# Performance work log

Measured on AMD Instinct MI355X. Metric: run time of the kernel, lower is better.

The kernel has to match this reference:

```python
import jax, jax.numpy as jnp
import numpy as np

DIM = 1024
HIDDEN = 2048
NUM_EXPERTS = 8
TOP_K = 2


def setup_inputs() -> dict:
    key = jax.random.key(0)
    ks = jax.random.split(key, 6)
    scale = 0.02
    x = jax.random.normal(ks[0], (2, 4096, DIM), dtype=jnp.float32)
    # router: Linear(dim, num_experts, bias=False) -> weight [E, d]
    router_w = jax.random.normal(ks[1], (NUM_EXPERTS, DIM), dtype=jnp.float32) * scale
    # per-expert MLP: Linear(d, h) -> w1 [E, h, d], b1 [E, h]; Linear(h, d) -> w2 [E, d, h], b2 [E, d]
    w1 = jax.random.normal(ks[2], (NUM_EXPERTS, HIDDEN, DIM), dtype=jnp.float32) * scale
    b1 = jnp.zeros((NUM_EXPERTS, HIDDEN), dtype=jnp.float32)
    w2 = jax.random.normal(ks[3], (NUM_EXPERTS, DIM, HIDDEN), dtype=jnp.float32) * scale
    b2 = jnp.zeros((NUM_EXPERTS, DIM), dtype=jnp.float32)
    return {"x": x, "router_w": router_w, "w1": w1, "b1": b1, "w2": w2, "b2": b2}


def reference(x, router_w, w1, b1, w2, b2):
    b, s, d = x.shape
    xf = x.reshape(-1, d)                              # [T, d]
    logits = xf @ router_w.T                           # [T, E]
    all_probs = jax.nn.softmax(logits, axis=-1)
    topk_logits, topk_inds = jax.lax.top_k(logits, TOP_K)   # [T, K]
    topk_probs = jax.nn.softmax(topk_logits, axis=-1)
    E = router_w.shape[0]
    onehot = jax.nn.one_hot(topk_inds, E, dtype=xf.dtype)   # [T, K, E]
    # combine weights per (token, expert); zero where expert not selected
    gate = jnp.einsum('tke,tk->te', onehot, topk_probs)     # [T, E]
    # load-balancing auxiliary loss
    f_i = onehot.mean(axis=(0, 1))                          # [E]
    P_i = all_probs.mean(axis=0)                            # [E]
    aux_loss = E * jnp.sum(f_i * P_i)
    # dense per-expert MLP, weighted combine (dropout=0 / eval mode)
    out = jnp.zeros_like(xf)
    for e in range(E):  # fixed small loop over experts
        h = jax.nn.gelu(xf @ w1[e].T + b1[e], approximate=False)  # exact GELU (torch default)
        y = h @ w2[e].T + b2[e]
        out = out + gate[:, e:e + 1] * y
    return out.reshape(b, s, d), aux_loss
```

## Files before the change

kernel.cpp:

```cpp
#include <hip/hip_runtime.h>


#define TOKS 8192
#define DIMD 1024
#define HID  2048
#define NE   8

#define OFF_COUNTS   0
#define OFF_OFFSETS  64
#define OFF_CURSORS  128
#define OFF_TILEOFF  192
#define OFF_TOPKI    256
#define OFF_TOPKG    (OFF_TOPKI + TOKS*2*4)
#define OFF_BLKPS    (OFF_TOPKG + TOKS*2*4)
#define OFF_ATOK     (OFF_BLKPS + 2048*NE*4)
#define OFF_AGATE    (OFF_ATOK + TOKS*2*4)
#define OFF_PINV     (OFF_AGATE + TOKS*2*4)
#define OFF_XG       (1u << 20)
#define XG_ROWS      (TOKS*2 + 256)
#define OFF_W1B      (OFF_XG  + (size_t)XG_ROWS * DIMD * 2)
#define OFF_W2B      (OFF_W1B + (size_t)NE * HID * DIMD * 2)
#define OFF_H        (OFF_W2B + (size_t)NE * DIMD * HID * 2)
#define OFF_Y        (OFF_H   + (size_t)XG_ROWS * HID * 2)

typedef __bf16 bf16x8 __attribute__((ext_vector_type(8)));
typedef float  floatx4 __attribute__((ext_vector_type(4)));

__device__ __forceinline__ float bf2f(unsigned short u) {
    return __uint_as_float(((unsigned)u) << 16);
}
__device__ __forceinline__ unsigned short f2bf(float f) {
    unsigned u = __float_as_uint(f);
    unsigned r = (u + 0x7FFFu + ((u >> 16) & 1u)) >> 16;
    return (unsigned short)r;
}

#define GLOBAL_AS(p) ((const __attribute__((address_space(1))) unsigned int*)(p))
#define LDS_AS(p)    ((__attribute__((address_space(3))) unsigned int*)(p))

__device__ __forceinline__ int xcd_remap(int bid, int nwg) {
    int xcd = bid & 7, pos = bid >> 3;
    int q = nwg >> 3, r = nwg & 7;
    int start = (xcd < r) ? xcd * (q + 1) : r * (q + 1) + (xcd - r) * q;
    return start + pos;
}

__global__ void convert_w_kernel(const float4* __restrict__ w1,
                                 ushort4* __restrict__ w1b, int n1,
                                 const float4* __restrict__ w2,
                                 ushort4* __restrict__ w2b, int n2) {
    int i = blockIdx.x * blockDim.x + threadIdx.x;
    int stride = gridDim.x * blockDim.x;
    int ntot = n1 + n2;
    for (; i < ntot; i += stride) {
        float4 v; ushort4 o;
        if (i < n1) v = w1[i]; else v = w2[i - n1];
        o.x = f2bf(v.x); o.y = f2bf(v.y); o.z = f2bf(v.z); o.w = f2bf(v.w);
        if (i < n1) w1b[i] = o; else w2b[i - n1] = o;
    }
}

__global__ __launch_bounds__(256) void router_kernel(
    const float* __restrict__ x, const float* __restrict__ rw,
    int* __restrict__ topki, float* __restrict__ topkg,
    float* __restrict__ blkps)
{
    int wave = threadIdx.x >> 6;
    int lane = threadIdx.x & 63;
    int t = blockIdx.x * 4 + wave;
    const float* xt = x + (size_t)t * DIMD;

    float acc[NE];
#pragma unroll
    for (int e = 0; e < NE; e++) acc[e] = 0.f;
    for (int i = 0; i < DIMD / 64; i++) {
        float xv = xt[lane + 64 * i];
#pragma unroll
        for (int e = 0; e < NE; e++) acc[e] += xv * rw[e * DIMD + lane + 64 * i];
    }
#pragma unroll
    for (int off = 32; off > 0; off >>= 1) {
#pragma unroll
        for (int e = 0; e < NE; e++) acc[e] += __shfl_down(acc[e], off);
    }

    __shared__ float ps[4][NE];
    if (lane == 0) {
        float m = acc[0];
#pragma unroll
        for (int e = 1; e < NE; e++) m = fmaxf(m, acc[e]);
        float ex[NE], s = 0.f;
#pragma unroll
        for (int e = 0; e < NE; e++) { ex[e] = expf(acc[e] - m); s += ex[e]; }
        float inv = 1.f / s;
#pragma unroll
        for (int e = 0; e < NE; e++) ps[wave][e] = ex[e] * inv;

        int i0 = 0; float l0 = acc[0];
#pragma unroll
        for (int e = 1; e < NE; e++) if (acc[e] > l0) { l0 = acc[e]; i0 = e; }
        int i1 = -1; float l1 = -3.4e38f;
#pragma unroll
        for (int e = 0; e < NE; e++) if (e != i0 && acc[e] > l1) { l1 = acc[e]; i1 = e; }
        float e1 = expf(l1 - l0);
        float g0 = 1.f / (1.f + e1);
        float g1 = e1 * g0;
        topki[t * 2 + 0] = i0; topki[t * 2 + 1] = i1;
        topkg[t * 2 + 0] = g0; topkg[t * 2 + 1] = g1;
    }
    __syncthreads();
    if (threadIdx.x < NE) {
        float s = ps[0][threadIdx.x] + ps[1][threadIdx.x] + ps[2][threadIdx.x] + ps[3][threadIdx.x];
        blkps[blockIdx.x * NE + threadIdx.x] = s;
    }
}

__global__ __launch_bounds__(256) void finalize_kernel(
    const int* __restrict__ topki, const float* __restrict__ blkps,
    int* __restrict__ counts, int* __restrict__ offsets, int* __restrict__ cursors,
    int* __restrict__ tileoff, float* __restrict__ aux_out)
{
    __shared__ float psum[NE];
    __shared__ int cnt[NE];
    int tid = threadIdx.x;
    if (tid < NE) { psum[tid] = 0.f; cnt[tid] = 0; }
    __syncthreads();

    float lp[NE]; int lc[NE];
#pragma unroll
    for (int e = 0; e < NE; e++) { lp[e] = 0.f; lc[e] = 0; }
    const float4* bp4 = (const float4*)blkps;
    for (int i = tid; i < 2048 * NE / 4; i += 256) {
        float4 v = bp4[i];
        int eb = (4 * i) & 7;
        lp[eb + 0] += v.x; lp[eb + 1] += v.y; lp[eb + 2] += v.z; lp[eb + 3] += v.w;
    }
    const int4* ti4 = (const int4*)topki;
    for (int i = tid; i < TOKS * 2 / 4; i += 256) {
        int4 v = ti4[i];
        lc[v.x]++; lc[v.y]++; lc[v.z]++; lc[v.w]++;
    }
#pragma unroll
    for (int e = 0; e < NE; e++) { atomicAdd(&psum[e], lp[e]); atomicAdd(&cnt[e], lc[e]); }
    __syncthreads();

    if (tid == 0) {
        int off = 0, to = 0;
        for (int e = 0; e < NE; e++) {
            counts[e] = cnt[e];
            offsets[e] = off; cursors[e] = off;
            tileoff[e] = to;
            off += cnt[e];
            to += (cnt[e] + 255) >> 8;
        }
        offsets[NE] = off; tileoff[NE] = to;
        float aux = 0.f;
        for (int e = 0; e < NE; e++)
            aux += ((float)cnt[e] / (float)(TOKS * 2)) * (psum[e] / (float)TOKS);
        aux_out[0] = (float)NE * aux;
    }
}

__global__ __launch_bounds__(64) void fill_kernel(
    const int* __restrict__ topki, const float* __restrict__ topkg,
    int* __restrict__ cursors, int* __restrict__ atok, float* __restrict__ agate,
    int* __restrict__ posinv)
{
    int lane = threadIdx.x;
    int t = blockIdx.x * 64 + lane;
    unsigned long long below = (lane == 63) ? 0x7FFFFFFFFFFFFFFFull
                                            : ((1ull << lane) - 1ull);
#pragma unroll
    for (int k = 0; k < 2; k++) {
        int e = topki[t * 2 + k];
        float g = topkg[t * 2 + k];
        for (int ee = 0; ee < NE; ee++) {
            bool pred = (e == ee);
            unsigned long long mask = __ballot(pred ? 1 : 0);
            if (mask) {
                int leader = __ffsll((unsigned long long)mask) - 1;
                int base = 0;
                if (lane == leader) base = atomicAdd(&cursors[ee], (int)__popcll(mask));
                base = __shfl(base, leader);
                if (pred) {
                    int pos = base + (int)__popcll(mask & below);
                    atok[pos] = t;
                    agate[pos] = g;
                    posinv[t * 2 + k] = pos;
                }
            }
        }
    }
}

__global__ __launch_bounds__(256) void gather_x_kernel(
    const float* __restrict__ x, const int* __restrict__ atok,
    ushort* __restrict__ Xg)
{
    int r = blockIdx.x;
    int tid = threadIdx.x;
    int tok = atok[r];
    float4 v = ((const float4*)(x + (size_t)tok * DIMD))[tid];
    ushort4 o;
    o.x = f2bf(v.x); o.y = f2bf(v.y); o.z = f2bf(v.z); o.w = f2bf(v.w);
    ((ushort4*)(Xg + (size_t)r * DIMD))[tid] = o;
}

template<int LD, int NT>
__device__ __forceinline__ void gemm8ph(
    const ushort* __restrict__ gApanel, const ushort* __restrict__ gBpanel,
    ushort (&lds)[2][64][512], floatx4 (&acc)[8][4],
    int lane, int wave, int wr, int wc, int l15, int quad)
{
    const bf16x8* C0 = (const bf16x8*)&lds[0][0][0];
    const bf16x8* C1 = (const bf16x8*)&lds[1][0][0];

    auto stage_half = [&](int bsel, int hf, int u) {
        const ushort* panel = (hf & 2) ? gBpanel : gApanel;
        int rbase = (hf & 1) * 128 + wave * 16 + l15;
        const ushort* s0 = panel + (size_t)rbase * LD + u * 64 + quad * 8;
        __builtin_amdgcn_global_load_lds(GLOBAL_AS(s0),
            LDS_AS(&lds[bsel][hf * 16 + wave * 2 + 0][0]), 16, 0, 0);
        __builtin_amdgcn_global_load_lds(GLOBAL_AS(s0 + 32),
            LDS_AS(&lds[bsel][hf * 16 + wave * 2 + 1][0]), 16, 0, 0);
    };

#pragma unroll
    for (int i = 0; i < 8; i++)
#pragma unroll
        for (int j = 0; j < 4; j++) acc[i][j] = (floatx4){0.f, 0.f, 0.f, 0.f};

    bf16x8 af[4][2], bf[2][2];

#define PH(CB, MH, NH, RA, RB, DOSTAGE, SB, SHF, SU, DOWAIT, DEEP)            \
    {                                                                          \
        if (RA) {                                                              \
            _Pragma("unroll") for (int mi = 0; mi < 4; mi++) {                 \
                af[mi][0] = CB[((wr * 8 + (MH)*4 + mi) * 2 + 0) * 64 + lane];  \
                af[mi][1] = CB[((wr * 8 + (MH)*4 + mi) * 2 + 1) * 64 + lane];  \
            }                                                                  \
        }                                                                      \
        if (RB) {                                                              \
            _Pragma("unroll") for (int nj = 0; nj < 2; nj++) {                 \
                bf[nj][0] = CB[(32 + (wc * 4 + (NH)*2 + nj) * 2 + 0) * 64 + lane]; \
                bf[nj][1] = CB[(32 + (wc * 4 + (NH)*2 + nj) * 2 + 1) * 64 + lane]; \
            }                                                                  \
        }                                                                      \
        if (DOSTAGE) stage_half(SB, SHF, SU);                                  \
        __builtin_amdgcn_s_barrier();                                          \
        asm volatile("s_waitcnt lgkmcnt(0)" ::: "memory");                     \
        __builtin_amdgcn_sched_barrier(0);                                     \
        __builtin_amdgcn_s_setprio(1);                                         \
        _Pragma("unroll") for (int mi = 0; mi < 4; mi++)                       \
            _Pragma("unroll") for (int nj = 0; nj < 2; nj++)                   \
                _Pragma("unroll") for (int kk = 0; kk < 2; kk++)               \
                    acc[(MH)*4 + mi][(NH)*2 + nj] =                            \
                        __builtin_amdgcn_mfma_f32_16x16x32_bf16(               \
                            af[mi][kk], bf[nj][kk],                            \
                            acc[(MH)*4 + mi][(NH)*2 + nj], 0, 0, 0);           \
        __builtin_amdgcn_s_setprio(0);                                         \
        if (DOWAIT) {                                                          \
            if (DEEP) asm volatile("s_waitcnt vmcnt(0)" ::: "memory");         \
            else      asm volatile("s_waitcnt vmcnt(4)" ::: "memory");         \
        }                                                                      \
        __builtin_amdgcn_s_barrier();                                          \
    }

    stage_half(0, 0, 0);
    stage_half(0, 2, 0);
    stage_half(0, 3, 0);
    stage_half(0, 1, 0);
    stage_half(1, 0, 1);
    stage_half(1, 3, 1);
    asm volatile("s_waitcnt vmcnt(4)" ::: "memory");
    __builtin_amdgcn_s_barrier();

    for (int u = 0; u < NT; u += 2) {
        PH(C0, 0, 0, 1, 1, (u + 1 < NT), 1, 1, u + 1, 0, 0);
        PH(C0, 0, 1, 0, 1, (u + 1 < NT), 1, 2, u + 1, 0, 0);
        PH(C0, 1, 1, 1, 0, (u + 2 < NT), 0, 0, u + 2, 0, 0);
        PH(C0, 1, 0, 0, 1, (u + 2 < NT), 0, 3, u + 2, 1, (u + 2 >= NT));
        PH(C1, 0, 0, 1, 1, (u + 2 < NT), 0, 1, u + 2, 0, 0);
        PH(C1, 0, 1, 0, 1, (u + 2 < NT), 0, 2, u + 2, 0, 0);
        PH(C1, 1, 1, 1, 0, (u + 3 < NT), 1, 0, u + 3, 0, 0);
        PH(C1, 1, 0, 0, 1, (u + 3 < NT), 1, 3, u + 3, 1, (u + 3 >= NT));
    }
#undef PH
}

__global__ __launch_bounds__(512, 2) void phase1_kernel(
    const ushort* __restrict__ Xg, const ushort* __restrict__ w1b,
    const float* __restrict__ b1,
    const int* __restrict__ counts, const int* __restrict__ offsets,
    const int* __restrict__ tileoff, unsigned short* __restrict__ Hbuf)
{
    const int NCOLT = HID / 256;
    int total = tileoff[NE] * NCOLT;
    int idx = xcd_remap((int)blockIdx.x, (int)gridDim.x);
    if (idx >= total) return;
    int ct = idx & (NCOLT - 1);
    int rowt = idx / NCOLT;
    int e = 0;
    while (rowt >= tileoff[e + 1]) e++;
    int row0 = (rowt - tileoff[e]) * 256;
    int cnt = counts[e];
    int base = offsets[e];
    int colbase = ct * 256;

    __shared__ ushort lds[2][64][512];

    int tid = threadIdx.x;
    int lane = tid & 63;
    int wave = tid >> 6;
    int wr = wave >> 2, wc = wave & 3;
    int l15 = lane & 15, quad = lane >> 4;

    const ushort* gApanel = Xg + (size_t)(base + row0) * DIMD;
    const ushort* gBpanel = w1b + (size_t)e * HID * DIMD + (size_t)colbase * DIMD;

    floatx4 acc[8][4];
    gemm8ph<DIMD, DIMD / 64>(gApanel, gBpanel, lds, acc, lane, wave, wr, wc, l15, quad);

    float b1v[4];
#pragma unroll
    for (int j = 0; j < 4; j++)
        b1v[j] = b1[e * HID + colbase + 64 * wc + 16 * j + l15];
#pragma unroll
    for (int i = 0; i < 8; i++) {
#pragma unroll
        for (int rr = 0; rr < 4; rr++) {
            int pr = row0 + 128 * wr + 16 * i + quad * 4 + rr;
            if (pr < cnt) {
                size_t hrow = (size_t)(base + pr) * HID;
#pragma unroll
                for (int j = 0; j < 4; j++) {
                    int col = colbase + 64 * wc + 16 * j + l15;
                    float v = acc[i][j][rr] + b1v[j];
                    v = 0.5f * v * (1.f + erff(v * 0.70710678118654752f));
                    Hbuf[hrow + col] = f2bf(v);
                }
            }
        }
    }
}

__global__ __launch_bounds__(512, 2) void phase2_kernel(
    const ushort* __restrict__ Hbuf, const ushort* __restrict__ w2b,
    const int* __restrict__ counts, const int* __restrict__ offsets,
    const int* __restrict__ tileoff, ushort* __restrict__ Y)
{
    const int NCOLT = DIMD / 256;
    int total = tileoff[NE] * NCOLT;
    int idx = xcd_remap((int)blockIdx.x, (int)gridDim.x);
    if (idx >= total) return;
    int ct = idx & (NCOLT - 1);
    int rowt = idx / NCOLT;
    int e = 0;
    while (rowt >= tileoff[e + 1]) e++;
    int row0 = (rowt - tileoff[e]) * 256;
    int cnt = counts[e];
    int base = offsets[e];
    int colbase = ct * 256;

    __shared__ ushort lds[2][64][512];

    int tid = threadIdx.x;
    int lane = tid & 63;
    int wave = tid >> 6;
    int wr = wave >> 2, wc = wave & 3;
    int l15 = lane & 15, quad = lane >> 4;

    const ushort* gApanel = Hbuf + (size_t)(base + row0) * HID;
    const ushort* gBpanel = w2b + (size_t)e * DIMD * HID + (size_t)colbase * HID;

    floatx4 acc[8][4];
    gemm8ph<HID, HID / 64>(gApanel, gBpanel, lds, acc, lane, wave, wr, wc, l15, quad);

#pragma unroll
    for (int i = 0; i < 8; i++) {
#pragma unroll
        for (int rr = 0; rr < 4; rr++) {
            int pr = row0 + 128 * wr + 16 * i + quad * 4 + rr;
            if (pr < cnt) {
                size_t yrow = (size_t)(base + pr) * DIMD;
#pragma unroll
                for (int j = 0; j < 4; j++) {
                    int col = colbase + 64 * wc + 16 * j + l15;
                    Y[yrow + col] = f2bf(acc[i][j][rr]);
                }
            }
        }
    }
}

__global__ __launch_bounds__(256) void combine_kernel(
    const ushort* __restrict__ Y, const float* __restrict__ b2,
    const int* __restrict__ topki, const float* __restrict__ topkg,
    const int* __restrict__ posinv, float* __restrict__ out)
{
    int wave = threadIdx.x >> 6;
    int lane = threadIdx.x & 63;
    int t = blockIdx.x * 4 + wave;
    int e0 = topki[t * 2 + 0], e1 = topki[t * 2 + 1];
    float g0 = topkg[t * 2 + 0], g1 = topkg[t * 2 + 1];
    int p0 = posinv[t * 2 + 0], p1 = posinv[t * 2 + 1];

    const ushort4* y0 = (const ushort4*)(Y + (size_t)p0 * DIMD);
    const ushort4* y1 = (const ushort4*)(Y + (size_t)p1 * DIMD);
    const float4* b20 = (const float4*)(b2 + (size_t)e0 * DIMD);
    const float4* b21 = (const float4*)(b2 + (size_t)e1 * DIMD);
    float4* o4 = (float4*)(out + (size_t)t * DIMD);

#pragma unroll
    for (int c = 0; c < DIMD / 4 / 64; c++) {
        int i = lane + 64 * c;
        ushort4 a = y0[i], b = y1[i];
        float4 ba = b20[i], bb = b21[i];
        float4 r;
        r.x = g0 * (bf2f(a.x) + ba.x) + g1 * (bf2f(b.x) + bb.x);
        r.y = g0 * (bf2f(a.y) + ba.y) + g1 * (bf2f(b.y) + bb.y);
        r.z = g0 * (bf2f(a.z) + ba.z) + g1 * (bf2f(b.z) + bb.z);
        r.w = g0 * (bf2f(a.w) + ba.w) + g1 * (bf2f(b.w) + bb.w);
        o4[i] = r;
    }
}

extern "C" void kernel_launch(void* const* d_in, const int* in_sizes, int n_in,
                              void* d_out, int out_size, void* d_ws, size_t ws_size,
                              hipStream_t stream) {
    const float* x  = (const float*)d_in[0];
    const float* rw = (const float*)d_in[1];
    const float* w1 = (const float*)d_in[2];
    const float* b1 = (const float*)d_in[3];
    const float* w2 = (const float*)d_in[4];
    const float* b2 = (const float*)d_in[5];
    float* out = (float*)d_out;

    char* ws = (char*)d_ws;
    int*   counts  = (int*)(ws + OFF_COUNTS);
    int*   offsets = (int*)(ws + OFF_OFFSETS);
    int*   cursors = (int*)(ws + OFF_CURSORS);
    int*   tileoff = (int*)(ws + OFF_TILEOFF);
    int*   topki   = (int*)(ws + OFF_TOPKI);
    float* topkg   = (float*)(ws + OFF_TOPKG);
    float* blkps   = (float*)(ws + OFF_BLKPS);
    int*   atok    = (int*)(ws + OFF_ATOK);
    float* agate   = (float*)(ws + OFF_AGATE);
    int*   posinv  = (int*)(ws + OFF_PINV);
    ushort* Xg     = (ushort*)(ws + OFF_XG);
    ushort* w1b    = (ushort*)(ws + OFF_W1B);
    ushort* w2b    = (ushort*)(ws + OFF_W2B);
    ushort* Hbuf   = (ushort*)(ws + OFF_H);
    ushort* Y      = (ushort*)(ws + OFF_Y);

    convert_w_kernel<<<8192, 256, 0, stream>>>(
        (const float4*)w1, (ushort4*)w1b, NE * HID * DIMD / 4,
        (const float4*)w2, (ushort4*)w2b, NE * DIMD * HID / 4);

    router_kernel<<<TOKS / 4, 256, 0, stream>>>(x, rw, topki, topkg, blkps);
    finalize_kernel<<<1, 256, 0, stream>>>(topki, blkps, counts, offsets, cursors,
                                           tileoff, out + (size_t)TOKS * DIMD);
    fill_kernel<<<TOKS / 64, 64, 0, stream>>>(topki, topkg, cursors, atok, agate,
                                              posinv);
    gather_x_kernel<<<TOKS * 2, 256, 0, stream>>>(x, atok, Xg);

    phase1_kernel<<<71 * (HID / 256), 512, 0, stream>>>(
        Xg, w1b, b1, counts, offsets, tileoff, Hbuf);
    phase2_kernel<<<71 * (DIMD / 256), 512, 0, stream>>>(
        Hbuf, w2b, counts, offsets, tileoff, Y);
    combine_kernel<<<TOKS / 4, 256, 0, stream>>>(Y, b2, topki, topkg, posinv, out);
}
```

Baseline: 591.3 us.

## Restage GEMM LDS loads by fragment units to prefetch deeper and drop lgkm waits

Changes how the 8-phase bf16 MFMA GEMM stages A/B tiles into LDS. Tiles are now staged in fragment-aligned units, so each phase's prefetch frees and refills exactly the rows it finished consuming. One more unit is prefetched up front (vmcnt 4→6), and the explicit lgkmcnt(0) wait and sched_barrier before the MFMAs are replaced with compiler memory fences. This aims to overlap global loads with compute more deeply and cut stall points, at the risk of LDS read/write hazards if the new unit ordering or wait counts are wrong.

Result: no change. 582.2 us (-1.5%).

```diff
diff --git a/kernel.cpp b/kernel.cpp
--- a/kernel.cpp
+++ b/kernel.cpp
@@ -37,6 +37,7 @@
 
 #define GLOBAL_AS(p) ((const __attribute__((address_space(1))) unsigned int*)(p))
 #define LDS_AS(p)    ((__attribute__((address_space(3))) unsigned int*)(p))
+#define CFENCE()     asm volatile("" ::: "memory")
 
 __device__ __forceinline__ int xcd_remap(int bid, int nwg) {
     int xcd = bid & 7, pos = bid >> 3;
@@ -215,14 +216,23 @@
     const bf16x8* C0 = (const bf16x8*)&lds[0][0][0];
     const bf16x8* C1 = (const bf16x8*)&lds[1][0][0];
 
-    auto stage_half = [&](int bsel, int hf, int u) {
-        const ushort* panel = (hf & 2) ? gBpanel : gApanel;
-        int rbase = (hf & 1) * 128 + wave * 16 + l15;
-        const ushort* s0 = panel + (size_t)rbase * LD + u * 64 + quad * 8;
+    auto stage_unit = [&](int bsel, int unit, int u) {
+        int s, chunk;
+        const ushort* panel;
+        if (unit < 2) {
+            s = (wave < 4 ? wave : wave + 4) + unit * 4;
+            chunk = s * 2;
+            panel = gApanel;
+        } else {
+            s = (wave & 1) + ((wave >> 1) * 4) + ((unit == 3) ? 2 : 0);
+            chunk = 32 + s * 2;
+            panel = gBpanel;
+        }
+        const ushort* s0 = panel + (size_t)(s * 16 + l15) * LD + u * 64 + quad * 8;
         __builtin_amdgcn_global_load_lds(GLOBAL_AS(s0),
-            LDS_AS(&lds[bsel][hf * 16 + wave * 2 + 0][0]), 16, 0, 0);
+            LDS_AS(&lds[bsel][chunk + 0][0]), 16, 0, 0);
         __builtin_amdgcn_global_load_lds(GLOBAL_AS(s0 + 32),
-            LDS_AS(&lds[bsel][hf * 16 + wave * 2 + 1][0]), 16, 0, 0);
+            LDS_AS(&lds[bsel][chunk + 1][0]), 16, 0, 0);
     };
 
 #pragma unroll
@@ -232,24 +242,24 @@
 
     bf16x8 af[4][2], bf[2][2];
 
-#define PH(CB, MH, NH, RA, RB, DOSTAGE, SB, SHF, SU, DOWAIT, DEEP)            \
+#define PH(CB, MH, NH, RA, RB, DOSTAGE, SB, SUNIT, SU, DOWAIT, DEEP)          \
     {                                                                          \
+        if (RB) {                                                              \
+            _Pragma("unroll") for (int nj = 0; nj < 2; nj++) {                 \
+                bf[nj][0] = CB[(32 + (wc * 4 + (NH)*2 + nj) * 2 + 0) * 64 + lane]; \
+                bf[nj][1] = CB[(32 + (wc * 4 + (NH)*2 + nj) * 2 + 1) * 64 + lane]; \
+            }                                                                  \
+        }                                                                      \
         if (RA) {                                                              \
             _Pragma("unroll") for (int mi = 0; mi < 4; mi++) {                 \
                 af[mi][0] = CB[((wr * 8 + (MH)*4 + mi) * 2 + 0) * 64 + lane];  \
                 af[mi][1] = CB[((wr * 8 + (MH)*4 + mi) * 2 + 1) * 64 + lane];  \
             }                                                                  \
         }                                                                      \
-        if (RB) {                                                              \
-            _Pragma("unroll") for (int nj = 0; nj < 2; nj++) {                 \
-                bf[nj][0] = CB[(32 + (wc * 4 + (NH)*2 + nj) * 2 + 0) * 64 + lane]; \
-                bf[nj][1] = CB[(32 + (wc * 4 + (NH)*2 + nj) * 2 + 1) * 64 + lane]; \
-            }                                                                  \
-        }                                                                      \
-        if (DOSTAGE) stage_half(SB, SHF, SU);                                  \
+        if (DOSTAGE) stage_unit(SB, SUNIT, SU);                                \
+        CFENCE();                                                              \
         __builtin_amdgcn_s_barrier();                                          \
-        asm volatile("s_waitcnt lgkmcnt(0)" ::: "memory");                     \
-        __builtin_amdgcn_sched_barrier(0);                                     \
+        CFENCE();                                                              \
         __builtin_amdgcn_s_setprio(1);                                         \
         _Pragma("unroll") for (int mi = 0; mi < 4; mi++)                       \
             _Pragma("unroll") for (int nj = 0; nj < 2; nj++)                   \
@@ -261,29 +271,34 @@
         __builtin_amdgcn_s_setprio(0);                                         \
         if (DOWAIT) {                                                          \
             if (DEEP) asm volatile("s_waitcnt vmcnt(0)" ::: "memory");         \
-            else      asm volatile("s_waitcnt vmcnt(4)" ::: "memory");         \
+            else      asm volatile("s_waitcnt vmcnt(6)" ::: "memory");         \
         }                                                                      \
+        CFENCE();                                                              \
         __builtin_amdgcn_s_barrier();                                          \
-    }
-
-    stage_half(0, 0, 0);
-    stage_half(0, 2, 0);
-    stage_half(0, 3, 0);
-    stage_half(0, 1, 0);
-    stage_half(1, 0, 1);
-    stage_half(1, 3, 1);
-    asm volatile("s_waitcnt vmcnt(4)" ::: "memory");
+        CFENCE();                                                              \
+    }
+
+    stage_unit(0, 0, 0);
+    stage_unit(0, 2, 0);
+    stage_unit(0, 3, 0);
+    stage_unit(0, 1, 0);
+    stage_unit(1, 0, 1);
+    stage_unit(1, 3, 1);
+    stage_unit(1, 1, 1);
+    asm volatile("s_waitcnt vmcnt(6)" ::: "memory");
+    CFENCE();
     __builtin_amdgcn_s_barrier();
+    CFENCE();
 
     for (int u = 0; u < NT; u += 2) {
-        PH(C0, 0, 0, 1, 1, (u + 1 < NT), 1, 1, u + 1, 0, 0);
-        PH(C0, 0, 1, 0, 1, (u + 1 < NT), 1, 2, u + 1, 0, 0);
-        PH(C0, 1, 1, 1, 0, (u + 2 < NT), 0, 0, u + 2, 0, 0);
-        PH(C0, 1, 0, 0, 1, (u + 2 < NT), 0, 3, u + 2, 1, (u + 2 >= NT));
-        PH(C1, 0, 0, 1, 1, (u + 2 < NT), 0, 1, u + 2, 0, 0);
-        PH(C1, 0, 1, 0, 1, (u + 2 < NT), 0, 2, u + 2, 0, 0);
-        PH(C1, 1, 1, 1, 0, (u + 3 < NT), 1, 0, u + 3, 0, 0);
-        PH(C1, 1, 0, 0, 1, (u + 3 < NT), 1, 3, u + 3, 1, (u + 3 >= NT));
+        PH(C0, 0, 0, 1, 1, (u + 1 < NT), 1, 2, u + 1, 0, 0);
+        PH(C0, 0, 1, 0, 1, (u + 2 < NT), 0, 0, u + 2, 0, 0);
+        PH(C0, 1, 1, 1, 0, (u + 2 < NT), 0, 3, u + 2, 0, 0);
+        PH(C0, 1, 0, 0, 1, (u + 2 < NT), 0, 1, u + 2, 1, (u + 2 >= NT));
+        PH(C1, 0, 0, 1, 1, (u + 2 < NT), 0, 2, u + 2, 0, 0);
+        PH(C1, 0, 1, 0, 1, (u + 3 < NT), 1, 0, u + 3, 0, 0);
+        PH(C1, 1, 1, 1, 0, (u + 3 < NT), 1, 3, u + 3, 0, 0);
+        PH(C1, 1, 0, 0, 1, (u + 3 < NT), 1, 1, u + 3, 1, (u + 3 >= NT));
     }
 #undef PH
 }
```

## Replace 8-phase GEMM pipeline with one fat phase per K-tile

Applied to the files above, without the earlier changes.

Replaces the eight-phase ping-pong schedule, where LDS fragment reads, half-tile staging and MFMA bursts were interleaved with a barrier pair per phase, with a simpler loop. Each K-tile now reads all A and B fragments at once, issues the full stage of tile u+2, then runs 64 MFMAs. This cuts the number of barriers per K-tile from 16 to 2 and lengthens the MFMA bursts. In exchange it needs more fragment registers (8x2 + 4x2 bf16x8), which puts the launch bound of 2 blocks per CU at risk. It also loses the finer overlap between LDS reads and compute across the two waves.

Result: no change. 593.1 us (+0.3%).

```diff
diff --git a/kernel.cpp b/kernel.cpp
--- a/kernel.cpp
+++ b/kernel.cpp
@@ -207,22 +207,26 @@
 }
 
 template<int LD, int NT>
-__device__ __forceinline__ void gemm8ph(
+__device__ __forceinline__ void gemm_fat(
     const ushort* __restrict__ gApanel, const ushort* __restrict__ gBpanel,
     ushort (&lds)[2][64][512], floatx4 (&acc)[8][4],
     int lane, int wave, int wr, int wc, int l15, int quad)
 {
-    const bf16x8* C0 = (const bf16x8*)&lds[0][0][0];
-    const bf16x8* C1 = (const bf16x8*)&lds[1][0][0];
-
-    auto stage_half = [&](int bsel, int hf, int u) {
-        const ushort* panel = (hf & 2) ? gBpanel : gApanel;
-        int rbase = (hf & 1) * 128 + wave * 16 + l15;
-        const ushort* s0 = panel + (size_t)rbase * LD + u * 64 + quad * 8;
-        __builtin_amdgcn_global_load_lds(GLOBAL_AS(s0),
-            LDS_AS(&lds[bsel][hf * 16 + wave * 2 + 0][0]), 16, 0, 0);
-        __builtin_amdgcn_global_load_lds(GLOBAL_AS(s0 + 32),
-            LDS_AS(&lds[bsel][hf * 16 + wave * 2 + 1][0]), 16, 0, 0);
+    auto stage_tile = [&](int bsel, int u) {
+#pragma unroll
+        for (int t = 0; t < 2; t++) {
+            int s = wave * 2 + t;
+            const ushort* a0 = gApanel + (size_t)(s * 16 + l15) * LD + u * 64 + quad * 8;
+            __builtin_amdgcn_global_load_lds(GLOBAL_AS(a0),
+                LDS_AS(&lds[bsel][s * 2 + 0][0]), 16, 0, 0);
+            __builtin_amdgcn_global_load_lds(GLOBAL_AS(a0 + 32),
+                LDS_AS(&lds[bsel][s * 2 + 1][0]), 16, 0, 0);
+            const ushort* b0 = gBpanel + (size_t)(s * 16 + l15) * LD + u * 64 + quad * 8;
+            __builtin_amdgcn_global_load_lds(GLOBAL_AS(b0),
+                LDS_AS(&lds[bsel][32 + s * 2 + 0][0]), 16, 0, 0);
+            __builtin_amdgcn_global_load_lds(GLOBAL_AS(b0 + 32),
+                LDS_AS(&lds[bsel][32 + s * 2 + 1][0]), 16, 0, 0);
+        }
     };
 
 #pragma unroll
@@ -230,62 +234,48 @@
 #pragma unroll
         for (int j = 0; j < 4; j++) acc[i][j] = (floatx4){0.f, 0.f, 0.f, 0.f};
 
-    bf16x8 af[4][2], bf[2][2];
-
-#define PH(CB, MH, NH, RA, RB, DOSTAGE, SB, SHF, SU, DOWAIT, DEEP)            \
-    {                                                                          \
-        if (RA) {                                                              \
-            _Pragma("unroll") for (int mi = 0; mi < 4; mi++) {                 \
-                af[mi][0] = CB[((wr * 8 + (MH)*4 + mi) * 2 + 0) * 64 + lane];  \
-                af[mi][1] = CB[((wr * 8 + (MH)*4 + mi) * 2 + 1) * 64 + lane];  \
-            }                                                                  \
-        }                                                                      \
-        if (RB) {                                                              \
-            _Pragma("unroll") for (int nj = 0; nj < 2; nj++) {                 \
-                bf[nj][0] = CB[(32 + (wc * 4 + (NH)*2 + nj) * 2 + 0) * 64 + lane]; \
-                bf[nj][1] = CB[(32 + (wc * 4 + (NH)*2 + nj) * 2 + 1) * 64 + lane]; \
-            }                                                                  \
-        }                                                                      \
-        if (DOSTAGE) stage_half(SB, SHF, SU);                                  \
-        __builtin_amdgcn_s_barrier();                                          \
-        asm volatile("s_waitcnt lgkmcnt(0)" ::: "memory");                     \
-        __builtin_amdgcn_sched_barrier(0);                                     \
-        __builtin_amdgcn_s_setprio(1);                                         \
-        _Pragma("unroll") for (int mi = 0; mi < 4; mi++)                       \
-            _Pragma("unroll") for (int nj = 0; nj < 2; nj++)                   \
-                _Pragma("unroll") for (int kk = 0; kk < 2; kk++)               \
-                    acc[(MH)*4 + mi][(NH)*2 + nj] =                            \
-                        __builtin_amdgcn_mfma_f32_16x16x32_bf16(               \
-                            af[mi][kk], bf[nj][kk],                            \
-                            acc[(MH)*4 + mi][(NH)*2 + nj], 0, 0, 0);           \
-        __builtin_amdgcn_s_setprio(0);                                         \
-        if (DOWAIT) {                                                          \
-            if (DEEP) asm volatile("s_waitcnt vmcnt(0)" ::: "memory");         \
-            else      asm volatile("s_waitcnt vmcnt(4)" ::: "memory");         \
-        }                                                                      \
-        __builtin_amdgcn_s_barrier();                                          \
-    }
-
-    stage_half(0, 0, 0);
-    stage_half(0, 2, 0);
-    stage_half(0, 3, 0);
-    stage_half(0, 1, 0);
-    stage_half(1, 0, 1);
-    stage_half(1, 3, 1);
-    asm volatile("s_waitcnt vmcnt(4)" ::: "memory");
+    stage_tile(0, 0);
+    stage_tile(1, 1);
+    asm volatile("s_waitcnt vmcnt(8)");
     __builtin_amdgcn_s_barrier();
-
-    for (int u = 0; u < NT; u += 2) {
-        PH(C0, 0, 0, 1, 1, (u + 1 < NT), 1, 1, u + 1, 0, 0);
-        PH(C0, 0, 1, 0, 1, (u + 1 < NT), 1, 2, u + 1, 0, 0);
-        PH(C0, 1, 1, 1, 0, (u + 2 < NT), 0, 0, u + 2, 0, 0);
-        PH(C0, 1, 0, 0, 1, (u + 2 < NT), 0, 3, u + 2, 1, (u + 2 >= NT));
-        PH(C1, 0, 0, 1, 1, (u + 2 < NT), 0, 1, u + 2, 0, 0);
-        PH(C1, 0, 1, 0, 1, (u + 2 < NT), 0, 2, u + 2, 0, 0);
-        PH(C1, 1, 1, 1, 0, (u + 3 < NT), 1, 0, u + 3, 0, 0);
-        PH(C1, 1, 0, 0, 1, (u + 3 < NT), 1, 3, u + 3, 1, (u + 3 >= NT));
-    }
-#undef PH
+    __builtin_amdgcn_sched_barrier(0);
+
+    for (int u = 0; u < NT; u++) {
+        const bf16x8* C = (const bf16x8*)&lds[u & 1][0][0];
+        bf16x8 af[8][2], bfr[4][2];
+#pragma unroll
+        for (int mi = 0; mi < 8; mi++) {
+            af[mi][0] = C[((wr * 8 + mi) * 2 + 0) * 64 + lane];
+            af[mi][1] = C[((wr * 8 + mi) * 2 + 1) * 64 + lane];
+        }
+#pragma unroll
+        for (int nj = 0; nj < 4; nj++) {
+            bfr[nj][0] = C[(32 + (wc * 4 + nj) * 2 + 0) * 64 + lane];
+            bfr[nj][1] = C[(32 + (wc * 4 + nj) * 2 + 1) * 64 + lane];
+        }
+        __builtin_amdgcn_sched_barrier(0);
+        asm volatile("s_waitcnt lgkmcnt(0)");
+        __builtin_amdgcn_s_barrier();
+        __builtin_amdgcn_sched_barrier(0);
+        if (u + 2 < NT) stage_tile(u & 1, u + 2);
+        __builtin_amdgcn_s_setprio(1);
+#pragma unroll
+        for (int mi = 0; mi < 8; mi++)
+#pragma unroll
+            for (int nj = 0; nj < 4; nj++) {
+                acc[mi][nj] = __builtin_amdgcn_mfma_f32_16x16x32_bf16(
+                    af[mi][0], bfr[nj][0], acc[mi][nj], 0, 0, 0);
+                acc[mi][nj] = __builtin_amdgcn_mfma_f32_16x16x32_bf16(
+                    af[mi][1], bfr[nj][1], acc[mi][nj], 0, 0, 0);
+            }
+        __builtin_amdgcn_s_setprio(0);
+        if (u + 1 < NT) {
+            if (u + 2 < NT) asm volatile("s_waitcnt vmcnt(8)");
+            else            asm volatile("s_waitcnt vmcnt(0)");
+        }
+        __builtin_amdgcn_s_barrier();
+        __builtin_amdgcn_sched_barrier(0);
+    }
 }
 
 __global__ __launch_bounds__(512, 2) void phase1_kernel(
@@ -319,7 +309,7 @@
     const ushort* gBpanel = w1b + (size_t)e * HID * DIMD + (size_t)colbase * DIMD;
 
     floatx4 acc[8][4];
-    gemm8ph<DIMD, DIMD / 64>(gApanel, gBpanel, lds, acc, lane, wave, wr, wc, l15, quad);
+    gemm_fat<DIMD, DIMD / 64>(gApanel, gBpanel, lds, acc, lane, wave, wr, wc, l15, quad);
 
     float b1v[4];
 #pragma unroll
@@ -374,7 +364,7 @@
     const ushort* gBpanel = w2b + (size_t)e * DIMD * HID + (size_t)colbase * HID;
 
     floatx4 acc[8][4];
-    gemm8ph<HID, HID / 64>(gApanel, gBpanel, lds, acc, lane, wave, wr, wc, l15, quad);
+    gemm_fat<HID, HID / 64>(gApanel, gBpanel, lds, acc, lane, wave, wr, wc, l15, quad);
 
 #pragma unroll
     for (int i = 0; i < 8; i++) {
```
